# Performance work log

Hardware: AMD Instinct MI355X
Metric: run time of the kernel (lower is better)

The kernel has to match this reference:

```python
import jax, jax.numpy as jnp
import numpy as np

N = 100000      # hits
P = 512         # particle ids (0 = noise, skipped)
D = 8           # condensation-space dim
Q_MIN = 0.01
REPULSION_SCALING = 10.0


def setup_inputs() -> dict:
    key = jax.random.key(0)
    k1, k2, k3, k4, k5 = jax.random.split(key, 5)
    w = jax.random.normal(k1, (N,), dtype=jnp.float32)
    # beta in (0, 0.95) so arctanh stays well-conditioned
    beta = jax.random.uniform(k2, (N,), dtype=jnp.float32) * 0.95
    x = jax.random.normal(k3, (N, D), dtype=jnp.float32)
    y = jax.random.normal(k4, (N,), dtype=jnp.float32)
    particle_id = jax.random.randint(k5, (N,), 0, P)
    return {"w": w, "beta": beta, "x": x, "y": y, "particle_id": particle_id}


def _safe_sqrt(s):
    # sqrt with zero (sub)gradient at 0, matching torch.norm's behavior at 0
    pos = s > 0
    return jnp.where(pos, jnp.sqrt(jnp.where(pos, s, 1.0)), 0.0)


def _condensation_loss(beta, x, particle_id):
    n = beta.shape[0]
    q = jnp.arctanh(beta) ** 2 + Q_MIN                     # [N]
    # per-particle condensation point: hit with max q (torch.argmax -> first)
    q_max = jax.ops.segment_max(q, particle_id, num_segments=P)          # [P]
    counts = jax.ops.segment_sum(jnp.ones_like(q), particle_id, num_segments=P)
    is_max = q == q_max[particle_id]
    cand = jnp.where(is_max, jnp.arange(n), n)
    alpha_idx = jnp.clip(jax.ops.segment_min(cand, particle_id, num_segments=P), 0, n - 1)
    valid = (counts > 0) & (jnp.arange(P) != 0)            # skip noise pid 0 and absent pids
    q_alpha = jnp.where(valid, q_max, 0.0)                 # [P], sanitized (-inf for empty segs)
    x_alpha = x[alpha_idx]                                  # [P, D]
    # squared distances [N, P] via GEMM (avoids [N, P, D] intermediate)
    sq = (jnp.sum(x * x, axis=1, keepdims=True)
          - 2.0 * (x @ x_alpha.T)
          + jnp.sum(x_alpha * x_alpha, axis=1)[None, :])
    sq = jnp.maximum(sq, 0.0)
    dist = _safe_sqrt(sq)
    va = sq * q_alpha[None, :]                              # attractive potential
    vr = jnp.maximum(1.0 - dist, 0.0) * q_alpha[None, :]    # repulsive hinge
    M = (particle_id[:, None] == jnp.arange(P)[None, :]).astype(x.dtype)  # [N, P]
    per_p = jnp.mean(q[:, None] * (M * va + REPULSION_SCALING * (1.0 - M) * vr), axis=0)  # [P]
    return jnp.sum(jnp.where(valid, per_p, 0.0))


def reference(w, beta, x, y, particle_id):
    return _condensation_loss(beta, x, particle_id)
```

## Files before the change

### kernel.cpp

```cpp
#include <hip/hip_runtime.h>

#define P_IDS 512
#define DIM 8
#define QMIN 0.01f
#define REP 10.0f
#define TBLS 64
#define CHUNK 64
#define NCHUNK (P_IDS / CHUNK)
#define HPT 4
#define HB (256 * HPT)

typedef unsigned long long ull;

__launch_bounds__(256)
__global__ void stageA_kernel(const float* __restrict__ beta,
                              const int* __restrict__ pid,
                              float* __restrict__ q_out,
                              ull* __restrict__ tables,
                              float* __restrict__ out,
                              int n) {
    __shared__ ull s_keys[P_IDS];
    s_keys[threadIdx.x] = 0ULL;
    s_keys[threadIdx.x + 256] = 0ULL;
    __syncthreads();
    for (int i = blockIdx.x * 256 + threadIdx.x; i < n; i += TBLS * 256) {
        float b = beta[i];
        float at = 0.5f * logf((1.0f + b) / (1.0f - b));
        float qv = fmaf(at, at, QMIN);
        q_out[i] = qv;
        ull key = ((ull)__float_as_uint(qv) << 32) |
                  (ull)(unsigned int)(~(unsigned int)i);
        atomicMax(&s_keys[pid[i]], key);
    }
    __syncthreads();
    ull* dst = tables + (size_t)blockIdx.x * P_IDS;
    dst[threadIdx.x] = s_keys[threadIdx.x];
    dst[threadIdx.x + 256] = s_keys[threadIdx.x + 256];
    if (blockIdx.x == 0 && threadIdx.x == 0) out[0] = 0.0f;
}

__launch_bounds__(256)
__global__ void loss_kernel(const float* __restrict__ x,
                            const float* __restrict__ q,
                            const int* __restrict__ pid,
                            const ull* __restrict__ tables,
                            float* __restrict__ out,
                            int n) {
    __shared__ ull    s_part[4][CHUNK];
    __shared__ float  s_xa[CHUNK * DIM];
    __shared__ float2 s_meta[CHUNK];
    __shared__ float  s_red[4];

    const int tid  = threadIdx.x;
    const int wave = tid >> 6, lane = tid & 63;
    const int chunk = blockIdx.x & (NCHUNK - 1);
    const int hb    = blockIdx.x / NCHUNK;
    const int p0    = chunk * CHUNK;

    ull k = 0ULL;
#pragma unroll
    for (int t = wave; t < TBLS; t += 4) {
        ull v = tables[(size_t)t * P_IDS + p0 + lane];
        k = (v > k) ? v : k;
    }
    s_part[wave][lane] = k;
    __syncthreads();
    if (tid < CHUNK) {
        k = s_part[0][tid];
        ull v1 = s_part[1][tid], v2 = s_part[2][tid], v3 = s_part[3][tid];
        k = (v1 > k) ? v1 : k; k = (v2 > k) ? v2 : k; k = (v3 > k) ? v3 : k;
        bool valid = (k != 0ULL) && ((p0 + tid) != 0);
        float qa = valid ? __uint_as_float((unsigned int)(k >> 32)) : 0.0f;
        int idx = valid ? (int)(~(unsigned int)(k & 0xFFFFFFFFull)) : 0;
        float4 a0 = ((const float4*)x)[idx * 2];
        float4 a1 = ((const float4*)x)[idx * 2 + 1];
        float xa2 = a0.x * a0.x;
        xa2 = fmaf(a0.y, a0.y, xa2); xa2 = fmaf(a0.z, a0.z, xa2);
        xa2 = fmaf(a0.w, a0.w, xa2); xa2 = fmaf(a1.x, a1.x, xa2);
        xa2 = fmaf(a1.y, a1.y, xa2); xa2 = fmaf(a1.z, a1.z, xa2);
        xa2 = fmaf(a1.w, a1.w, xa2);
        ((float4*)s_xa)[tid * 2] = a0;
        ((float4*)s_xa)[tid * 2 + 1] = a1;
        s_meta[tid] = make_float2(qa, xa2);
    }
    __syncthreads();

    float xi[HPT][DIM], xi2[HPT], qi[HPT], acc[HPT];
    int   myj[HPT];
    int base = hb * HB + tid;
#pragma unroll
    for (int h = 0; h < HPT; ++h) {
        int i = base + h * 256;
        bool act = i < n;
        int ii = act ? i : 0;
        float4 v0 = ((const float4*)x)[ii * 2];
        float4 v1 = ((const float4*)x)[ii * 2 + 1];
        xi[h][0] = v0.x; xi[h][1] = v0.y; xi[h][2] = v0.z; xi[h][3] = v0.w;
        xi[h][4] = v1.x; xi[h][5] = v1.y; xi[h][6] = v1.z; xi[h][7] = v1.w;
        float s = 0.0f;
#pragma unroll
        for (int d = 0; d < DIM; ++d) s = fmaf(xi[h][d], xi[h][d], s);
        xi2[h] = s;
        qi[h]  = act ? q[ii] : 0.0f;
        myj[h] = act ? (pid[ii] - p0) : -1;
        acc[h] = 0.0f;
    }

    for (int j = 0; j < CHUNK; ++j) {
        float2 m  = s_meta[j];
        float4 a0 = ((const float4*)s_xa)[j * 2];
        float4 a1 = ((const float4*)s_xa)[j * 2 + 1];
        float sq[HPT];
#pragma unroll
        for (int h = 0; h < HPT; ++h) {
            float dot = xi[h][0] * a0.x;
            dot = fmaf(xi[h][1], a0.y, dot); dot = fmaf(xi[h][2], a0.z, dot);
            dot = fmaf(xi[h][3], a0.w, dot); dot = fmaf(xi[h][4], a1.x, dot);
            dot = fmaf(xi[h][5], a1.y, dot); dot = fmaf(xi[h][6], a1.z, dot);
            dot = fmaf(xi[h][7], a1.w, dot);
            sq[h] = fmaxf(fmaf(-2.0f, dot, xi2[h] + m.y), 0.0f);
        }
        float mn = fminf(fminf(sq[0], sq[1]), fminf(sq[2], sq[3]));
        if (__any(mn < 1.0f)) {
#pragma unroll
            for (int h = 0; h < HPT; ++h) {
                float vr = fmaxf(1.0f - __builtin_amdgcn_sqrtf(sq[h]), 0.0f);
                acc[h] = fmaf(vr, m.x, acc[h]);
            }
        }
    }

    float partial = 0.0f;
#pragma unroll
    for (int h = 0; h < HPT; ++h) {
        float t = REP * acc[h];
        int j = myj[h];
        if (j >= 0 && j < CHUNK) {
            float2 m = s_meta[j];
            float dot = xi[h][0] * s_xa[j * DIM + 0];
#pragma unroll
            for (int d = 1; d < DIM; ++d)
                dot = fmaf(xi[h][d], s_xa[j * DIM + d], dot);
            float sq = fmaxf(fmaf(-2.0f, dot, xi2[h] + m.y), 0.0f);
            float vr = fmaxf(1.0f - __builtin_amdgcn_sqrtf(sq), 0.0f);
            t += m.x * (sq - REP * vr);
        }
        partial = fmaf(qi[h], t, partial);
    }

#pragma unroll
    for (int off = 32; off > 0; off >>= 1)
        partial += __shfl_down(partial, off, 64);
    if ((tid & 63) == 0) s_red[tid >> 6] = partial;
    __syncthreads();
    if (tid == 0)
        atomicAdd(out, (s_red[0] + s_red[1] + s_red[2] + s_red[3]) / (float)n);
}

extern "C" void kernel_launch(void* const* d_in, const int* in_sizes, int n_in,
                              void* d_out, int out_size, void* d_ws, size_t ws_size,
                              hipStream_t stream) {
    int n = in_sizes[0];
    const float* beta = (const float*)d_in[1];
    const float* x    = (const float*)d_in[2];
    const int*   pid  = (const int*)d_in[4];
    float* out = (float*)d_out;

    char* ws = (char*)d_ws;
    size_t tab_bytes = ((size_t)TBLS * P_IDS * sizeof(ull) + 255) & ~(size_t)255;
    ull*   tables = (ull*)ws;
    float* q      = (float*)(ws + tab_bytes);

    stageA_kernel<<<TBLS, 256, 0, stream>>>(beta, pid, q, tables, out, n);
    int hit_blocks = (n + HB - 1) / HB;
    loss_kernel<<<hit_blocks * NCHUNK, 256, 0, stream>>>(x, q, pid, tables, out, n);
}
```

Baseline: 97.61 us.

## Replace per-block argmax tables with global atomics and use packed FMA dot products

```diff
diff --git a/kernel.cpp b/kernel.cpp
--- a/kernel.cpp
+++ b/kernel.cpp
@@ -4,72 +4,53 @@
 #define DIM 8
 #define QMIN 0.01f
 #define REP 10.0f
-#define TBLS 64
 #define CHUNK 64
 #define NCHUNK (P_IDS / CHUNK)
 #define HPT 4
 #define HB (256 * HPT)
 
 typedef unsigned long long ull;
+typedef float v2f __attribute__((ext_vector_type(2)));
 
 __launch_bounds__(256)
-__global__ void stageA_kernel(const float* __restrict__ beta,
-                              const int* __restrict__ pid,
-                              float* __restrict__ q_out,
-                              ull* __restrict__ tables,
-                              float* __restrict__ out,
-                              int n) {
-    __shared__ ull s_keys[P_IDS];
-    s_keys[threadIdx.x] = 0ULL;
-    s_keys[threadIdx.x + 256] = 0ULL;
-    __syncthreads();
-    for (int i = blockIdx.x * 256 + threadIdx.x; i < n; i += TBLS * 256) {
-        float b = beta[i];
-        float at = 0.5f * logf((1.0f + b) / (1.0f - b));
-        float qv = fmaf(at, at, QMIN);
-        q_out[i] = qv;
-        ull key = ((ull)__float_as_uint(qv) << 32) |
-                  (ull)(unsigned int)(~(unsigned int)i);
-        atomicMax(&s_keys[pid[i]], key);
-    }
-    __syncthreads();
-    ull* dst = tables + (size_t)blockIdx.x * P_IDS;
-    dst[threadIdx.x] = s_keys[threadIdx.x];
-    dst[threadIdx.x + 256] = s_keys[threadIdx.x + 256];
-    if (blockIdx.x == 0 && threadIdx.x == 0) out[0] = 0.0f;
+__global__ void q_kernel(const float* __restrict__ beta,
+                         const int* __restrict__ pid,
+                         float* __restrict__ q_out,
+                         ull* __restrict__ keys,
+                         float* __restrict__ out,
+                         int n) {
+    int i = blockIdx.x * 256 + threadIdx.x;
+    if (i == 0) out[0] = 0.0f;
+    if (i >= n) return;
+    float b = beta[i];
+    float at = 0.5f * logf((1.0f + b) / (1.0f - b));
+    float qv = fmaf(at, at, QMIN);
+    q_out[i] = qv;
+    ull key = ((ull)__float_as_uint(qv) << 32) |
+              (ull)(unsigned int)(~(unsigned int)i);
+    atomicMax(&keys[pid[i]], key);
 }
 
 __launch_bounds__(256)
 __global__ void loss_kernel(const float* __restrict__ x,
                             const float* __restrict__ q,
                             const int* __restrict__ pid,
-                            const ull* __restrict__ tables,
+                            const ull* __restrict__ keys,
                             float* __restrict__ out,
                             int n) {
-    __shared__ ull    s_part[4][CHUNK];
     __shared__ float  s_xa[CHUNK * DIM];
     __shared__ float2 s_meta[CHUNK];
     __shared__ float  s_red[4];
 
-    const int tid  = threadIdx.x;
-    const int wave = tid >> 6, lane = tid & 63;
+    const int tid   = threadIdx.x;
     const int chunk = blockIdx.x & (NCHUNK - 1);
     const int hb    = blockIdx.x / NCHUNK;
     const int p0    = chunk * CHUNK;
 
-    ull k = 0ULL;
-#pragma unroll
-    for (int t = wave; t < TBLS; t += 4) {
-        ull v = tables[(size_t)t * P_IDS + p0 + lane];
-        k = (v > k) ? v : k;
-    }
-    s_part[wave][lane] = k;
-    __syncthreads();
     if (tid < CHUNK) {
-        k = s_part[0][tid];
-        ull v1 = s_part[1][tid], v2 = s_part[2][tid], v3 = s_part[3][tid];
-        k = (v1 > k) ? v1 : k; k = (v2 > k) ? v2 : k; k = (v3 > k) ? v3 : k;
-        bool valid = (k != 0ULL) && ((p0 + tid) != 0);
+        int p = p0 + tid;
+        ull k = keys[p];
+        bool valid = (k != 0ULL) && (p != 0);
         float qa = valid ? __uint_as_float((unsigned int)(k >> 32)) : 0.0f;
         int idx = valid ? (int)(~(unsigned int)(k & 0xFFFFFFFFull)) : 0;
         float4 a0 = ((const float4*)x)[idx * 2];
@@ -85,7 +66,8 @@
     }
     __syncthreads();
 
-    float xi[HPT][DIM], xi2[HPT], qi[HPT], acc[HPT];
+    v2f   xiv[HPT][4];
+    float xi2[HPT], qi[HPT], acc[HPT];
     int   myj[HPT];
     int base = hb * HB + tid;
 #pragma unroll
@@ -95,11 +77,12 @@
         int ii = act ? i : 0;
         float4 v0 = ((const float4*)x)[ii * 2];
         float4 v1 = ((const float4*)x)[ii * 2 + 1];
-        xi[h][0] = v0.x; xi[h][1] = v0.y; xi[h][2] = v0.z; xi[h][3] = v0.w;
-        xi[h][4] = v1.x; xi[h][5] = v1.y; xi[h][6] = v1.z; xi[h][7] = v1.w;
-        float s = 0.0f;
-#pragma unroll
-        for (int d = 0; d < DIM; ++d) s = fmaf(xi[h][d], xi[h][d], s);
+        xiv[h][0] = (v2f){v0.x, v0.y}; xiv[h][1] = (v2f){v0.z, v0.w};
+        xiv[h][2] = (v2f){v1.x, v1.y}; xiv[h][3] = (v2f){v1.z, v1.w};
+        float s = v0.x * v0.x;
+        s = fmaf(v0.y, v0.y, s); s = fmaf(v0.z, v0.z, s); s = fmaf(v0.w, v0.w, s);
+        s = fmaf(v1.x, v1.x, s); s = fmaf(v1.y, v1.y, s); s = fmaf(v1.z, v1.z, s);
+        s = fmaf(v1.w, v1.w, s);
         xi2[h] = s;
         qi[h]  = act ? q[ii] : 0.0f;
         myj[h] = act ? (pid[ii] - p0) : -1;
@@ -110,14 +93,16 @@
         float2 m  = s_meta[j];
         float4 a0 = ((const float4*)s_xa)[j * 2];
         float4 a1 = ((const float4*)s_xa)[j * 2 + 1];
+        v2f b0 = (v2f){a0.x, a0.y}, b1 = (v2f){a0.z, a0.w};
+        v2f b2 = (v2f){a1.x, a1.y}, b3 = (v2f){a1.z, a1.w};
         float sq[HPT];
 #pragma unroll
         for (int h = 0; h < HPT; ++h) {
-            float dot = xi[h][0] * a0.x;
-            dot = fmaf(xi[h][1], a0.y, dot); dot = fmaf(xi[h][2], a0.z, dot);
-            dot = fmaf(xi[h][3], a0.w, dot); dot = fmaf(xi[h][4], a1.x, dot);
-            dot = fmaf(xi[h][5], a1.y, dot); dot = fmaf(xi[h][6], a1.z, dot);
-            dot = fmaf(xi[h][7], a1.w, dot);
+            v2f d = xiv[h][0] * b0;
+            d = __builtin_elementwise_fma(xiv[h][1], b1, d);
+            d = __builtin_elementwise_fma(xiv[h][2], b2, d);
+            d = __builtin_elementwise_fma(xiv[h][3], b3, d);
+            float dot = d.x + d.y;
             sq[h] = fmaxf(fmaf(-2.0f, dot, xi2[h] + m.y), 0.0f);
         }
         float mn = fminf(fminf(sq[0], sq[1]), fminf(sq[2], sq[3]));
@@ -137,10 +122,14 @@
         int j = myj[h];
         if (j >= 0 && j < CHUNK) {
             float2 m = s_meta[j];
-            float dot = xi[h][0] * s_xa[j * DIM + 0];
-#pragma unroll
-            for (int d = 1; d < DIM; ++d)
-                dot = fmaf(xi[h][d], s_xa[j * DIM + d], dot);
+            float dot = xiv[h][0].x * s_xa[j * DIM + 0];
+            dot = fmaf(xiv[h][0].y, s_xa[j * DIM + 1], dot);
+            dot = fmaf(xiv[h][1].x, s_xa[j * DIM + 2], dot);
+            dot = fmaf(xiv[h][1].y, s_xa[j * DIM + 3], dot);
+            dot = fmaf(xiv[h][2].x, s_xa[j * DIM + 4], dot);
+            dot = fmaf(xiv[h][2].y, s_xa[j * DIM + 5], dot);
+            dot = fmaf(xiv[h][3].x, s_xa[j * DIM + 6], dot);
+            dot = fmaf(xiv[h][3].y, s_xa[j * DIM + 7], dot);
             float sq = fmaxf(fmaf(-2.0f, dot, xi2[h] + m.y), 0.0f);
             float vr = fmaxf(1.0f - __builtin_amdgcn_sqrtf(sq), 0.0f);
             t += m.x * (sq - REP * vr);
@@ -167,11 +156,12 @@
     float* out = (float*)d_out;
 
     char* ws = (char*)d_ws;
-    size_t tab_bytes = ((size_t)TBLS * P_IDS * sizeof(ull) + 255) & ~(size_t)255;
-    ull*   tables = (ull*)ws;
-    float* q      = (float*)(ws + tab_bytes);
+    ull*   keys = (ull*)ws;
+    float* q    = (float*)(ws + 4096);
 
-    stageA_kernel<<<TBLS, 256, 0, stream>>>(beta, pid, q, tables, out, n);
+    hipMemsetAsync(keys, 0, P_IDS * sizeof(ull), stream);
+    int a_blocks = (n + 255) / 256;
+    q_kernel<<<a_blocks, 256, 0, stream>>>(beta, pid, q, keys, out, n);
     int hit_blocks = (n + HB - 1) / HB;
-    loss_kernel<<<hit_blocks * NCHUNK, 256, 0, stream>>>(x, q, pid, tables, out, n);
+    loss_kernel<<<hit_blocks * NCHUNK, 256, 0, stream>>>(x, q, pid, keys, out, n);
 }
```

Result: slower. 114.2 us (+17.0%).
